# Kernel optimization log

Measured on AMD Instinct MI355X. Metric: run time of the kernel, lower is better.

Reference implementation:

```python
import jax, jax.numpy as jnp
import numpy as np

D = 128       # in_features
H = 256       # hidden
OUT = 128     # out_features
NUM_STEPS = 3
K = 8         # k_neighbors (k = min(K, N))


def setup_inputs() -> dict:
    key = jax.random.key(0)
    ks = jax.random.split(key, 12)
    s = 0.02
    return {
        "x":    jax.random.normal(ks[0], (4, 4096, D), dtype=jnp.float32),
        # neighbor_proj: Linear(D -> H)
        "Wn":   jax.random.normal(ks[1], (D, H), dtype=jnp.float32) * s,
        "bn":   jnp.zeros((H,), dtype=jnp.float32),
        # local_rule[0]: Linear(D + H -> H)
        "W1":   jax.random.normal(ks[2], (D + H, H), dtype=jnp.float32) * s,
        "b1":   jnp.zeros((H,), dtype=jnp.float32),
        # local_rule[1]: LayerNorm(H)
        "ln_g": jnp.ones((H,), dtype=jnp.float32),
        "ln_b": jnp.zeros((H,), dtype=jnp.float32),
        # local_rule[3]: Linear(H -> D)
        "W2":   jax.random.normal(ks[3], (H, D), dtype=jnp.float32) * s,
        "b2":   jnp.zeros((D,), dtype=jnp.float32),
        # out_proj: Linear(D -> OUT)
        "Wo":   jax.random.normal(ks[4], (D, OUT), dtype=jnp.float32) * s,
        "bo":   jnp.zeros((OUT,), dtype=jnp.float32),
    }


def _layernorm(h, g, b, eps=1e-5):
    mu = jnp.mean(h, axis=-1, keepdims=True)
    var = jnp.var(h, axis=-1, keepdims=True)
    return (h - mu) * jax.lax.rsqrt(var + eps) * g + b


def reference(x, Wn, bn, W1, b1, ln_g, ln_b, W2, b2, Wo, bo):
    B, N, _ = x.shape
    k = min(K, N)
    batch_ix = jnp.arange(B)[:, None, None]  # (B,1,1)
    state = x
    for _ in range(NUM_STEPS):
        keys = state @ Wn + bn                                     # (B,N,H)
        keys = keys / jnp.maximum(
            jnp.linalg.norm(keys, axis=-1, keepdims=True), 1e-12)  # F.normalize
        sim = jnp.einsum('bnh,bmh->bnm', keys, keys)               # (B,N,N)
        _, idx = jax.lax.top_k(sim, k)                             # (B,N,k)
        gathered = state[batch_ix, idx]                            # (B,N,k,D)
        neighbor_agg = gathered.mean(axis=2) @ Wn + bn             # (B,N,H)
        combined = jnp.concatenate([state, neighbor_agg], axis=-1) # (B,N,D+H)
        h = _layernorm(combined @ W1 + b1, ln_g, ln_b)
        update = jax.nn.silu(h) @ W2 + b2                          # (B,N,D)
        state = state + update
    return state.mean(axis=1) @ Wo + bo                            # (B,OUT)
```

## Files before the change

kernel.cpp:

```cpp
#include <hip/hip_runtime.h>

#define DDIM 128
#define HDIM 256
#define BQ   4
#define NN   4096
#define RTOT (BQ*NN)

typedef short short8 __attribute__((ext_vector_type(8)));
typedef short short4v __attribute__((ext_vector_type(4)));
typedef float f32x16 __attribute__((ext_vector_type(16)));

__device__ inline unsigned short f2bf(float f) {
    unsigned int u = __float_as_uint(f);
    unsigned int r = (u + 0x7fffu + ((u >> 16) & 1u)) >> 16;
    return (unsigned short)r;
}
__device__ inline float bf2f(unsigned short h) {
    return __uint_as_float(((unsigned int)h) << 16);
}

#define MFMA32(a, b, c) __builtin_amdgcn_mfma_f32_32x32x16_bf16(a, b, c, 0, 0, 0)

__global__ void pack_w_kernel(const float* __restrict__ W, int N,
                              unsigned short* __restrict__ ph, unsigned short* __restrict__ pl) {
    int l = threadIdx.x, l31 = l & 31, lh = l >> 5;
    int nt = N >> 5;
    int t = blockIdx.x / nt, c = blockIdx.x % nt;
    short8 hv, lv;
#pragma unroll
    for (int j = 0; j < 8; ++j) {
        float f = W[(size_t)(t * 16 + lh * 8 + j) * N + c * 32 + l31];
        unsigned short h = f2bf(f);
        hv[j] = (short)h;
        lv[j] = (short)f2bf(f - bf2f(h));
    }
    *(short8*)(ph + (size_t)(blockIdx.x * 64 + l) * 8) = hv;
    *(short8*)(pl + (size_t)(blockIdx.x * 64 + l) * 8) = lv;
}

__global__ __launch_bounds__(256, 2)
void sim_topk_kernel(const unsigned short* __restrict__ khi,
                     const unsigned short* __restrict__ klo,
                     int* __restrict__ idxout) {
    __shared__ __align__(16) char smem[4 * 4 * 4096];

    const int id = blockIdx.x;
    const int xcd = id & 7;
    const int b = xcd >> 1;
    const int j = ((id >> 3) << 1) | (xcd & 1);
    const int rowbase = j * 32;
    const unsigned short* khiB = khi + (size_t)b * NN * HDIM;
    const unsigned short* kloB = klo + (size_t)b * NN * HDIM;

    const int tid = threadIdx.x;
    const int lane = tid & 63, w = tid >> 6;
    const int l31 = lane & 31, lh = lane >> 5;

    short8 ah[16], al[16];
    {
        const unsigned short* ph = khiB + (size_t)(rowbase + l31) * HDIM + lh * 8;
        const unsigned short* pl = kloB + (size_t)(rowbase + l31) * HDIM + lh * 8;
#pragma unroll
        for (int T = 0; T < 16; ++T) {
            ah[T] = *(const short8*)(ph + T * 16);
            al[T] = *(const short8*)(pl + T * 16);
        }
    }
#pragma unroll
    for (int T = 0; T < 16; ++T) {
        asm volatile("" : "+v"(ah[T]));
        asm volatile("" : "+v"(al[T]));
    }

    char* mybuf = smem + w * 16384;

    const int sc = lane >> 2, sg = lane & 3;
    const int ssw = (sg ^ ((sc >> 1) & 3)) * 8;
    auto stage = [&](int s) {
        const int cs2 = s >> 3, ks2 = s & 7;
        char* dst = mybuf + (s % 4) * 4096;
        const int c0 = w * 1024 + cs2 * 32;
#pragma unroll
        for (int p = 0; p < 2; ++p) {
            const unsigned short* pb = p ? kloB : khiB;
#pragma unroll
            for (int i = 0; i < 2; ++i) {
                const unsigned short* src = pb + (size_t)(c0 + i * 16 + sc) * HDIM + ks2 * 32 + ssw;
                __builtin_amdgcn_global_load_lds(
                    (const __attribute__((address_space(1))) void*)src,
                    (__attribute__((address_space(3))) void*)(dst + p * 2048 + i * 1024), 16, 0, 0);
            }
        }
    };

    stage(0);
    stage(1);
    stage(2);

    const int key = (l31 >> 1) & 3;
    const int rb0 = l31 * 64 + ((lh ^ key) * 16);
    const int rb1 = l31 * 64 + (((2 + lh) ^ key) * 16);

    float tv[8]; int ti[8];
#pragma unroll
    for (int s = 0; s < 8; ++s) { tv[s] = -1e30f; ti[s] = 0x7fffffff; }

    for (int cs = 0; cs < 32; ++cs) {
        f32x16 acc;
#pragma unroll
        for (int r = 0; r < 16; ++r) acc[r] = 0.f;

#pragma unroll
        for (int ks = 0; ks < 8; ++ks) {
            const int s = cs * 8 + ks;
            if (s < 254)       asm volatile("s_waitcnt vmcnt(8)" ::: "memory");
            else if (s == 254) asm volatile("s_waitcnt vmcnt(4)" ::: "memory");
            else               asm volatile("s_waitcnt vmcnt(0)" ::: "memory");

            const char* bufc = mybuf + (s % 4) * 4096;
            short8 Bh0 = *(const short8*)(bufc + rb0);
            short8 Bl0 = *(const short8*)(bufc + 2048 + rb0);
            short8 Bh1 = *(const short8*)(bufc + rb1);
            short8 Bl1 = *(const short8*)(bufc + 2048 + rb1);
            asm volatile("s_waitcnt lgkmcnt(4)" ::: "memory");
            if (s + 3 < 256) stage(s + 3);

            const int T0 = ks * 2, T1 = ks * 2 + 1;
            acc = MFMA32(Bh0, ah[T0], acc);
            acc = MFMA32(Bh0, al[T0], acc);
            acc = MFMA32(Bl0, ah[T0], acc);
            acc = MFMA32(Bh1, ah[T1], acc);
            acc = MFMA32(Bh1, al[T1], acc);
            acc = MFMA32(Bl1, ah[T1], acc);
        }

        const int cbase = w * 1024 + cs * 32 + 4 * lh;
#pragma unroll
        for (int r = 0; r < 16; ++r) {
            float v = acc[r];
            int col = cbase + (r & 3) + 8 * (r >> 2);
            if (v > tv[7]) {
                tv[7] = v; ti[7] = col;
#pragma unroll
                for (int q = 7; q >= 1; --q) {
                    if (tv[q] > tv[q - 1]) {
                        float a0 = tv[q]; tv[q] = tv[q - 1]; tv[q - 1] = a0;
                        int   c0_ = ti[q]; ti[q] = ti[q - 1]; ti[q - 1] = c0_;
                    }
                }
            }
        }
    }

    __syncthreads();
    float* vbuf = (float*)smem;
    int*   ibuf = (int*)(smem + 32 * 66 * 4);
    const int list = w * 2 + lh;
#pragma unroll
    for (int s = 0; s < 8; ++s) {
        vbuf[l31 * 66 + list * 8 + s] = tv[s];
        ibuf[l31 * 66 + list * 8 + s] = ti[s];
    }
    __syncthreads();
    if (tid < 32) {
        float fv[8]; int fi[8];
#pragma unroll
        for (int s = 0; s < 8; ++s) { fv[s] = -1e30f; fi[s] = 0x7fffffff; }
        for (int e = 0; e < 64; ++e) {
            float v = vbuf[tid * 66 + e];
            int  ix = ibuf[tid * 66 + e];
            bool ins = (v > fv[7]) || (v == fv[7] && ix < fi[7]);
            if (ins) {
                fv[7] = v; fi[7] = ix;
#pragma unroll
                for (int q = 7; q >= 1; --q) {
                    bool sw = (fv[q] > fv[q - 1]) || (fv[q] == fv[q - 1] && fi[q] < fi[q - 1]);
                    if (sw) {
                        float a0 = fv[q]; fv[q] = fv[q - 1]; fv[q - 1] = a0;
                        int   c0_ = fi[q]; fi[q] = fi[q - 1]; fi[q - 1] = c0_;
                    }
                }
            }
        }
        size_t basei = ((size_t)b * NN + rowbase + tid) * 8;
#pragma unroll
        for (int s = 0; s < 8; ++s) idxout[basei + s] = fi[s];
    }
}

__global__ __launch_bounds__(256, 2)
void gemm_keys_mfma(const float* __restrict__ A,
                    const unsigned short* __restrict__ wh, const unsigned short* __restrict__ wl,
                    const float* __restrict__ bias,
                    unsigned short* __restrict__ khi, unsigned short* __restrict__ klo) {
    __shared__ float ssqbuf[2][32][2];
    const int tid = threadIdx.x, lane = tid & 63, w = tid >> 6;
    const int l31 = lane & 31, lh = lane >> 5;
    const int rw = w & 1, cw = w >> 1;
    const int row = blockIdx.x * 64 + rw * 32 + l31;

    short8 ahi[8], alo[8];
    const float* ap = A + (size_t)row * DDIM + lh * 8;
#pragma unroll
    for (int T = 0; T < 8; ++T) {
        float4 f0 = *(const float4*)(ap + T * 16);
        float4 f1 = *(const float4*)(ap + T * 16 + 4);
        float ff[8] = {f0.x, f0.y, f0.z, f0.w, f1.x, f1.y, f1.z, f1.w};
#pragma unroll
        for (int j2 = 0; j2 < 8; ++j2) {
            unsigned short h = f2bf(ff[j2]);
            ahi[T][j2] = (short)h;
            alo[T][j2] = (short)f2bf(ff[j2] - bf2f(h));
        }
    }

    f32x16 acc[4];
#pragma unroll
    for (int ct = 0; ct < 4; ++ct)
#pragma unroll
        for (int r = 0; r < 16; ++r) acc[ct][r] = 0.f;

#pragma unroll
    for (int T = 0; T < 8; ++T) {
#pragma unroll
        for (int ct = 0; ct < 4; ++ct) {
            const size_t pi = (size_t)((T * 8 + cw * 4 + ct) * 64 + lane) * 8;
            short8 bh = *(const short8*)(wh + pi);
            short8 bl = *(const short8*)(wl + pi);
            acc[ct] = MFMA32(bh, ahi[T], acc[ct]);
            acc[ct] = MFMA32(bl, ahi[T], acc[ct]);
            acc[ct] = MFMA32(bh, alo[T], acc[ct]);
        }
    }

    float ss = 0.f;
#pragma unroll
    for (int ct = 0; ct < 4; ++ct)
#pragma unroll
        for (int g = 0; g < 4; ++g) {
            const int c0 = cw * 128 + ct * 32 + g * 8 + lh * 4;
            float4 bz = *(const float4*)(bias + c0);
            float bzf[4] = {bz.x, bz.y, bz.z, bz.w};
#pragma unroll
            for (int j2 = 0; j2 < 4; ++j2) {
                acc[ct][g * 4 + j2] += bzf[j2];
                ss += acc[ct][g * 4 + j2] * acc[ct][g * 4 + j2];
            }
        }
    ss += __shfl_xor(ss, 32);
    if (lh == 0) ssqbuf[rw][l31][cw] = ss;
    __syncthreads();
    float sstot = ssqbuf[rw][l31][0] + ssqbuf[rw][l31][1];
    float scn = 1.0f / fmaxf(sqrtf(sstot), 1e-12f);

#pragma unroll
    for (int ct = 0; ct < 4; ++ct)
#pragma unroll
        for (int g = 0; g < 4; ++g) {
            const int c0 = cw * 128 + ct * 32 + g * 8 + lh * 4;
            short4v hv, lv;
#pragma unroll
            for (int j2 = 0; j2 < 4; ++j2) {
                float vn = acc[ct][g * 4 + j2] * scn;
                unsigned short h = f2bf(vn);
                hv[j2] = (short)h;
                lv[j2] = (short)f2bf(vn - bf2f(h));
            }
            *(short4v*)(khi + (size_t)row * HDIM + c0) = hv;
            *(short4v*)(klo + (size_t)row * HDIM + c0) = lv;
        }
}

__global__ __launch_bounds__(256, 2)
void gemm_agg_mfma(const float* __restrict__ A,
                   const unsigned short* __restrict__ wh, const unsigned short* __restrict__ wl,
                   const float* __restrict__ bias,
                   unsigned short* __restrict__ oh, unsigned short* __restrict__ ol) {
    const int tid = threadIdx.x, lane = tid & 63, w = tid >> 6;
    const int l31 = lane & 31, lh = lane >> 5;
    const int rw = w & 1, cw = w >> 1;
    const int row = blockIdx.x * 64 + rw * 32 + l31;

    short8 ahi[8], alo[8];
    const float* ap = A + (size_t)row * DDIM + lh * 8;
#pragma unroll
    for (int T = 0; T < 8; ++T) {
        float4 f0 = *(const float4*)(ap + T * 16);
        float4 f1 = *(const float4*)(ap + T * 16 + 4);
        float ff[8] = {f0.x, f0.y, f0.z, f0.w, f1.x, f1.y, f1.z, f1.w};
#pragma unroll
        for (int j2 = 0; j2 < 8; ++j2) {
            unsigned short h = f2bf(ff[j2]);
            ahi[T][j2] = (short)h;
            alo[T][j2] = (short)f2bf(ff[j2] - bf2f(h));
        }
    }

    f32x16 acc[4];
#pragma unroll
    for (int ct = 0; ct < 4; ++ct)
#pragma unroll
        for (int r = 0; r < 16; ++r) acc[ct][r] = 0.f;

#pragma unroll
    for (int T = 0; T < 8; ++T) {
#pragma unroll
        for (int ct = 0; ct < 4; ++ct) {
            const size_t pi = (size_t)((T * 8 + cw * 4 + ct) * 64 + lane) * 8;
            short8 bh = *(const short8*)(wh + pi);
            short8 bl = *(const short8*)(wl + pi);
            acc[ct] = MFMA32(bh, ahi[T], acc[ct]);
            acc[ct] = MFMA32(bl, ahi[T], acc[ct]);
            acc[ct] = MFMA32(bh, alo[T], acc[ct]);
        }
    }

#pragma unroll
    for (int ct = 0; ct < 4; ++ct)
#pragma unroll
        for (int g = 0; g < 4; ++g) {
            const int c0 = cw * 128 + ct * 32 + g * 8 + lh * 4;
            float4 bz = *(const float4*)(bias + c0);
            float bzf[4] = {bz.x, bz.y, bz.z, bz.w};
            short4v hv, lv;
#pragma unroll
            for (int j2 = 0; j2 < 4; ++j2) {
                float vn = acc[ct][g * 4 + j2] + bzf[j2];
                unsigned short h = f2bf(vn);
                hv[j2] = (short)h;
                lv[j2] = (short)f2bf(vn - bf2f(h));
            }
            *(short4v*)(oh + (size_t)row * HDIM + c0) = hv;
            *(short4v*)(ol + (size_t)row * HDIM + c0) = lv;
        }
}

__global__ __launch_bounds__(256, 2)
void gemm_ln_mfma(const float* __restrict__ state,
                  const unsigned short* __restrict__ agh, const unsigned short* __restrict__ agl,
                  const unsigned short* __restrict__ wh, const unsigned short* __restrict__ wl,
                  const float* __restrict__ b1, const float* __restrict__ lng,
                  const float* __restrict__ lnb,
                  unsigned short* __restrict__ gh, unsigned short* __restrict__ gl) {
    __shared__ float s1buf[2][32][2], s2buf[2][32][2];
    const int tid = threadIdx.x, lane = tid & 63, w = tid >> 6;
    const int l31 = lane & 31, lh = lane >> 5;
    const int rw = w & 1, cw = w >> 1;
    const int row = blockIdx.x * 64 + rw * 32 + l31;

    f32x16 acc[4];
#pragma unroll
    for (int ct = 0; ct < 4; ++ct)
#pragma unroll
        for (int r = 0; r < 16; ++r) acc[ct][r] = 0.f;

    short8 ahi[8], alo[8];
    {
        const float* ap = state + (size_t)row * DDIM + lh * 8;
#pragma unroll
        for (int T = 0; T < 8; ++T) {
            float4 f0 = *(const float4*)(ap + T * 16);
            float4 f1 = *(const float4*)(ap + T * 16 + 4);
            float ff[8] = {f0.x, f0.y, f0.z, f0.w, f1.x, f1.y, f1.z, f1.w};
#pragma unroll
            for (int j2 = 0; j2 < 8; ++j2) {
                unsigned short h = f2bf(ff[j2]);
                ahi[T][j2] = (short)h;
                alo[T][j2] = (short)f2bf(ff[j2] - bf2f(h));
            }
        }
#pragma unroll
        for (int T = 0; T < 8; ++T)
#pragma unroll
            for (int ct = 0; ct < 4; ++ct) {
                const size_t pi = (size_t)((T * 8 + cw * 4 + ct) * 64 + lane) * 8;
                short8 bh = *(const short8*)(wh + pi);
                short8 bl = *(const short8*)(wl + pi);
                acc[ct] = MFMA32(bh, ahi[T], acc[ct]);
                acc[ct] = MFMA32(bl, ahi[T], acc[ct]);
                acc[ct] = MFMA32(bh, alo[T], acc[ct]);
            }
    }
#pragma unroll
    for (int kc = 1; kc < 3; ++kc) {
#pragma unroll
        for (int T = 0; T < 8; ++T) {
            ahi[T] = *(const short8*)(agh + (size_t)row * HDIM + (kc - 1) * 128 + T * 16 + lh * 8);
            alo[T] = *(const short8*)(agl + (size_t)row * HDIM + (kc - 1) * 128 + T * 16 + lh * 8);
        }
#pragma unroll
        for (int T = 0; T < 8; ++T)
#pragma unroll
            for (int ct = 0; ct < 4; ++ct) {
                const size_t pi = (size_t)(((kc * 8 + T) * 8 + cw * 4 + ct) * 64 + lane) * 8;
                short8 bh = *(const short8*)(wh + pi);
                short8 bl = *(const short8*)(wl + pi);
                acc[ct] = MFMA32(bh, ahi[T], acc[ct]);
                acc[ct] = MFMA32(bl, ahi[T], acc[ct]);
                acc[ct] = MFMA32(bh, alo[T], acc[ct]);
            }
    }

    float s1 = 0.f, s2 = 0.f;
#pragma unroll
    for (int ct = 0; ct < 4; ++ct)
#pragma unroll
        for (int g = 0; g < 4; ++g) {
            const int c0 = cw * 128 + ct * 32 + g * 8 + lh * 4;
            float4 bz = *(const float4*)(b1 + c0);
            float bzf[4] = {bz.x, bz.y, bz.z, bz.w};
#pragma unroll
            for (int j2 = 0; j2 < 4; ++j2) {
                acc[ct][g * 4 + j2] += bzf[j2];
                s1 += acc[ct][g * 4 + j2];
                s2 += acc[ct][g * 4 + j2] * acc[ct][g * 4 + j2];
            }
        }
    s1 += __shfl_xor(s1, 32);
    s2 += __shfl_xor(s2, 32);
    if (lh == 0) { s1buf[rw][l31][cw] = s1; s2buf[rw][l31][cw] = s2; }
    __syncthreads();
    float s1t = s1buf[rw][l31][0] + s1buf[rw][l31][1];
    float s2t = s2buf[rw][l31][0] + s2buf[rw][l31][1];
    float mu = s1t * (1.0f / HDIM);
    float var = s2t * (1.0f / HDIM) - mu * mu;
    float inv = 1.0f / sqrtf(var + 1e-5f);

#pragma unroll
    for (int ct = 0; ct < 4; ++ct)
#pragma unroll
        for (int g = 0; g < 4; ++g) {
            const int c0 = cw * 128 + ct * 32 + g * 8 + lh * 4;
            float4 gg = *(const float4*)(lng + c0);
            float4 bb = *(const float4*)(lnb + c0);
            float ggf[4] = {gg.x, gg.y, gg.z, gg.w};
            float bbf[4] = {bb.x, bb.y, bb.z, bb.w};
            short4v hv, lv;
#pragma unroll
            for (int j2 = 0; j2 < 4; ++j2) {
                float hval = (acc[ct][g * 4 + j2] - mu) * inv * ggf[j2] + bbf[j2];
                float gval = hval / (1.0f + expf(-hval));
                unsigned short h = f2bf(gval);
                hv[j2] = (short)h;
                lv[j2] = (short)f2bf(gval - bf2f(h));
            }
            *(short4v*)(gh + (size_t)row * HDIM + c0) = hv;
            *(short4v*)(gl + (size_t)row * HDIM + c0) = lv;
        }
}

__global__ __launch_bounds__(256, 2)
void gemm_upd_mfma(const unsigned short* __restrict__ gh, const unsigned short* __restrict__ gl,
                   const unsigned short* __restrict__ wh, const unsigned short* __restrict__ wl,
                   const float* __restrict__ b2, float* __restrict__ state) {
    const int tid = threadIdx.x, lane = tid & 63, w = tid >> 6;
    const int l31 = lane & 31, lh = lane >> 5;
    const int rw = w & 1, cw = w >> 1;
    const int row = blockIdx.x * 64 + rw * 32 + l31;

    f32x16 acc[2];
#pragma unroll
    for (int ct = 0; ct < 2; ++ct)
#pragma unroll
        for (int r = 0; r < 16; ++r) acc[ct][r] = 0.f;

    short8 ahi[8], alo[8];
#pragma unroll
    for (int kc = 0; kc < 2; ++kc) {
#pragma unroll
        for (int T = 0; T < 8; ++T) {
            ahi[T] = *(const short8*)(gh + (size_t)row * HDIM + kc * 128 + T * 16 + lh * 8);
            alo[T] = *(const short8*)(gl + (size_t)row * HDIM + kc * 128 + T * 16 + lh * 8);
        }
#pragma unroll
        for (int T = 0; T < 8; ++T)
#pragma unroll
            for (int ct = 0; ct < 2; ++ct) {
                const size_t pi = (size_t)(((kc * 8 + T) * 4 + cw * 2 + ct) * 64 + lane) * 8;
                short8 bh = *(const short8*)(wh + pi);
                short8 bl = *(const short8*)(wl + pi);
                acc[ct] = MFMA32(bh, ahi[T], acc[ct]);
                acc[ct] = MFMA32(bl, ahi[T], acc[ct]);
                acc[ct] = MFMA32(bh, alo[T], acc[ct]);
            }
    }

#pragma unroll
    for (int ct = 0; ct < 2; ++ct)
#pragma unroll
        for (int g = 0; g < 4; ++g) {
            const int c0 = cw * 64 + ct * 32 + g * 8 + lh * 4;
            float4 bz = *(const float4*)(b2 + c0);
            float bzf[4] = {bz.x, bz.y, bz.z, bz.w};
            float4* sp = (float4*)(state + (size_t)row * DDIM + c0);
            float4 sv = *sp;
            float svf[4] = {sv.x, sv.y, sv.z, sv.w};
#pragma unroll
            for (int j2 = 0; j2 < 4; ++j2) svf[j2] += acc[ct][g * 4 + j2] + bzf[j2];
            sv.x = svf[0]; sv.y = svf[1]; sv.z = svf[2]; sv.w = svf[3];
            *sp = sv;
        }
}

__global__ void gather_mean_kernel(const float* __restrict__ state, const int* __restrict__ idx,
                                   float* __restrict__ M) {
    __shared__ int ilds[16];
    int tid = threadIdx.x;
    int row0 = blockIdx.x * 2;
    if (tid < 16) ilds[tid] = idx[(size_t)row0 * 8 + tid];
    __syncthreads();
    int lr = tid >> 7, d = tid & 127;
    int grow = row0 + lr;
    int b = grow >> 12;
    const float* sb = state + (size_t)b * NN * DDIM;
    float acc = 0.f;
#pragma unroll
    for (int k = 0; k < 8; ++k) acc += sb[(size_t)ilds[lr * 8 + k] * DDIM + d];
    M[(size_t)grow * DDIM + d] = acc * 0.125f;
}

__global__ void partial_mean_kernel(const float* __restrict__ state, float* __restrict__ partial) {
    int b = blockIdx.y, seg = blockIdx.x, tid = threadIdx.x;
    const float* sp = state + ((size_t)b * NN + (size_t)seg * 128) * DDIM;
    float acc = 0.f;
    for (int i = 0; i < 128; ++i) acc += sp[(size_t)i * DDIM + tid];
    partial[((size_t)b * 32 + seg) * DDIM + tid] = acc;
}

__global__ void final_out_kernel(const float* __restrict__ partial, const float* __restrict__ Wo,
                                 const float* __restrict__ bo, float* __restrict__ out) {
    __shared__ float mean[BQ][DDIM];
    int tid = threadIdx.x;
    for (int o = tid; o < BQ * DDIM; o += 256) {
        int b = o >> 7, d = o & 127;
        float s = 0.f;
        for (int p = 0; p < 32; ++p) s += partial[((size_t)b * 32 + p) * DDIM + d];
        mean[b][d] = s * (1.0f / NN);
    }
    __syncthreads();
    for (int o = tid; o < BQ * DDIM; o += 256) {
        int b = o >> 7, c = o & 127;
        float acc = bo[c];
        for (int d = 0; d < DDIM; ++d) acc += mean[b][d] * Wo[d * DDIM + c];
        out[o] = acc;
    }
}

extern "C" void kernel_launch(void* const* d_in, const int* in_sizes, int n_in,
                              void* d_out, int out_size, void* d_ws, size_t ws_size,
                              hipStream_t stream) {
    const float* x   = (const float*)d_in[0];
    const float* Wn  = (const float*)d_in[1];
    const float* bn  = (const float*)d_in[2];
    const float* W1  = (const float*)d_in[3];
    const float* b1  = (const float*)d_in[4];
    const float* lng = (const float*)d_in[5];
    const float* lnb = (const float*)d_in[6];
    const float* W2  = (const float*)d_in[7];
    const float* b2  = (const float*)d_in[8];
    const float* Wo  = (const float*)d_in[9];
    const float* bo  = (const float*)d_in[10];
    float* out = (float*)d_out;

    float* ws    = (float*)d_ws;
    float* state = ws;
    unsigned short* agghi = (unsigned short*)(state + (size_t)RTOT * DDIM);
    unsigned short* agglo = agghi + (size_t)RTOT * HDIM;
    unsigned short* khi_b = agglo + (size_t)RTOT * HDIM;
    unsigned short* klo_b = khi_b + (size_t)RTOT * HDIM;
    float* Mbuf = (float*)khi_b;
    unsigned short* ghi = khi_b;
    unsigned short* glo = klo_b;
    float* partial = (float*)(klo_b + (size_t)RTOT * HDIM);
    int*   idxbuf  = (int*)(partial + (size_t)BQ * 32 * DDIM);
    unsigned short* wnh = (unsigned short*)(idxbuf + (size_t)RTOT * 8);
    unsigned short* wnl = wnh + 128 * 256;
    unsigned short* w1h = wnl + 128 * 256;
    unsigned short* w1l = w1h + 384 * 256;
    unsigned short* w2h = w1l + 384 * 256;
    unsigned short* w2l = w2h + 256 * 128;

    hipMemcpyAsync(state, x, (size_t)RTOT * DDIM * sizeof(float),
                   hipMemcpyDeviceToDevice, stream);

    pack_w_kernel<<<(128 / 16) * (256 / 32), 64, 0, stream>>>(Wn, 256, wnh, wnl);
    pack_w_kernel<<<(384 / 16) * (256 / 32), 64, 0, stream>>>(W1, 256, w1h, w1l);
    pack_w_kernel<<<(256 / 16) * (128 / 32), 64, 0, stream>>>(W2, 128, w2h, w2l);

    for (int step = 0; step < 3; ++step) {
        gemm_keys_mfma<<<RTOT / 64, 256, 0, stream>>>(state, wnh, wnl, bn, khi_b, klo_b);
        sim_topk_kernel<<<512, 256, 0, stream>>>(khi_b, klo_b, idxbuf);
        gather_mean_kernel<<<RTOT / 2, 256, 0, stream>>>(state, idxbuf, Mbuf);
        gemm_agg_mfma<<<RTOT / 64, 256, 0, stream>>>(Mbuf, wnh, wnl, bn, agghi, agglo);
        gemm_ln_mfma<<<RTOT / 64, 256, 0, stream>>>(state, agghi, agglo, w1h, w1l,
                                                    b1, lng, lnb, ghi, glo);
        gemm_upd_mfma<<<RTOT / 64, 256, 0, stream>>>(ghi, glo, w2h, w2l, b2, state);
    }
    partial_mean_kernel<<<dim3(32, BQ), 128, 0, stream>>>(state, partial);
    final_out_kernel<<<1, 256, 0, stream>>>(partial, Wo, bo, out);
}
```

Measured before the change: 832.2 us.

## Fuse gather-mean into aggregate GEMM and restage sim LDS tiles with 64-wide swizzle

Removes the separate gather_mean kernel and its M buffer round-trip. The aggregate GEMM now reads the eight neighbor indices per row and sums the neighbor state rows directly while building its bf16 hi/lo operands. Separately, the sim/top-k kernel's LDS staging is reorganized so that each stage loads either the hi or the lo half of a 64-wide k slab, using an 8-way XOR swizzle. Stages then alternate between 8 MFMAs (hi stage) and 4 MFMAs (lo stage) instead of 6 per stage. The fused gather adds scattered global reads inside the GEMM, and the new staging changes the load pipeline's balance.

After: 863.3 us. 3.7% more time.

```diff
diff --git a/kernel.cpp b/kernel.cpp
--- a/kernel.cpp
+++ b/kernel.cpp
@@ -74,22 +74,20 @@
 
     char* mybuf = smem + w * 16384;
 
-    const int sc = lane >> 2, sg = lane & 3;
-    const int ssw = (sg ^ ((sc >> 1) & 3)) * 8;
+    const int sc8 = lane >> 3, sg8 = lane & 7;
     auto stage = [&](int s) {
-        const int cs2 = s >> 3, ks2 = s & 7;
-        char* dst = mybuf + (s % 4) * 4096;
+        const int cs2 = s >> 3, sub = s & 7;
+        const int kb2 = sub >> 1;
+        const unsigned short* pb = (sub & 1) ? kloB : khiB;
+        char* dst = mybuf + (s & 3) * 4096;
         const int c0 = w * 1024 + cs2 * 32;
 #pragma unroll
-        for (int p = 0; p < 2; ++p) {
-            const unsigned short* pb = p ? kloB : khiB;
-#pragma unroll
-            for (int i = 0; i < 2; ++i) {
-                const unsigned short* src = pb + (size_t)(c0 + i * 16 + sc) * HDIM + ks2 * 32 + ssw;
-                __builtin_amdgcn_global_load_lds(
-                    (const __attribute__((address_space(1))) void*)src,
-                    (__attribute__((address_space(3))) void*)(dst + p * 2048 + i * 1024), 16, 0, 0);
-            }
+        for (int i = 0; i < 4; ++i) {
+            const unsigned short* src =
+                pb + (size_t)(c0 + i * 8 + sc8) * HDIM + kb2 * 64 + ((sg8 ^ sc8) * 8);
+            __builtin_amdgcn_global_load_lds(
+                (const __attribute__((address_space(1))) void*)src,
+                (__attribute__((address_space(3))) void*)(dst + i * 1024), 16, 0, 0);
         }
     };
 
@@ -97,9 +95,12 @@
     stage(1);
     stage(2);
 
-    const int key = (l31 >> 1) & 3;
-    const int rb0 = l31 * 64 + ((lh ^ key) * 16);
-    const int rb1 = l31 * 64 + (((2 + lh) ^ key) * 16);
+    const int key = l31 & 7;
+    const int rbase = l31 * 128;
+    const int sl0 = (((0) * 2 + lh) ^ key) * 16;
+    const int sl1 = (((1) * 2 + lh) ^ key) * 16;
+    const int sl2 = (((2) * 2 + lh) ^ key) * 16;
+    const int sl3 = (((3) * 2 + lh) ^ key) * 16;
 
     float tv[8]; int ti[8];
 #pragma unroll
@@ -111,27 +112,36 @@
         for (int r = 0; r < 16; ++r) acc[r] = 0.f;
 
 #pragma unroll
-        for (int ks = 0; ks < 8; ++ks) {
-            const int s = cs * 8 + ks;
+        for (int sub = 0; sub < 8; ++sub) {
+            const int s = cs * 8 + sub;
             if (s < 254)       asm volatile("s_waitcnt vmcnt(8)" ::: "memory");
             else if (s == 254) asm volatile("s_waitcnt vmcnt(4)" ::: "memory");
             else               asm volatile("s_waitcnt vmcnt(0)" ::: "memory");
 
-            const char* bufc = mybuf + (s % 4) * 4096;
-            short8 Bh0 = *(const short8*)(bufc + rb0);
-            short8 Bl0 = *(const short8*)(bufc + 2048 + rb0);
-            short8 Bh1 = *(const short8*)(bufc + rb1);
-            short8 Bl1 = *(const short8*)(bufc + 2048 + rb1);
+            const char* bufc = mybuf + (s & 3) * 4096;
+            short8 B0 = *(const short8*)(bufc + rbase + sl0);
+            short8 B1 = *(const short8*)(bufc + rbase + sl1);
+            short8 B2 = *(const short8*)(bufc + rbase + sl2);
+            short8 B3 = *(const short8*)(bufc + rbase + sl3);
             asm volatile("s_waitcnt lgkmcnt(4)" ::: "memory");
             if (s + 3 < 256) stage(s + 3);
 
-            const int T0 = ks * 2, T1 = ks * 2 + 1;
-            acc = MFMA32(Bh0, ah[T0], acc);
-            acc = MFMA32(Bh0, al[T0], acc);
-            acc = MFMA32(Bl0, ah[T0], acc);
-            acc = MFMA32(Bh1, ah[T1], acc);
-            acc = MFMA32(Bh1, al[T1], acc);
-            acc = MFMA32(Bl1, ah[T1], acc);
+            const int T0 = (sub >> 1) * 4;
+            if ((sub & 1) == 0) {
+                acc = MFMA32(B0, ah[T0],     acc);
+                acc = MFMA32(B0, al[T0],     acc);
+                acc = MFMA32(B1, ah[T0 + 1], acc);
+                acc = MFMA32(B1, al[T0 + 1], acc);
+                acc = MFMA32(B2, ah[T0 + 2], acc);
+                acc = MFMA32(B2, al[T0 + 2], acc);
+                acc = MFMA32(B3, ah[T0 + 3], acc);
+                acc = MFMA32(B3, al[T0 + 3], acc);
+            } else {
+                acc = MFMA32(B0, ah[T0],     acc);
+                acc = MFMA32(B1, ah[T0 + 1], acc);
+                acc = MFMA32(B2, ah[T0 + 2], acc);
+                acc = MFMA32(B3, ah[T0 + 3], acc);
+            }
         }
 
         const int cbase = w * 1024 + cs * 32 + 4 * lh;
@@ -272,7 +282,7 @@
 }
 
 __global__ __launch_bounds__(256, 2)
-void gemm_agg_mfma(const float* __restrict__ A,
+void gemm_agg_mfma(const float* __restrict__ state, const int* __restrict__ idx,
                    const unsigned short* __restrict__ wh, const unsigned short* __restrict__ wl,
                    const float* __restrict__ bias,
                    unsigned short* __restrict__ oh, unsigned short* __restrict__ ol) {
@@ -280,19 +290,32 @@
     const int l31 = lane & 31, lh = lane >> 5;
     const int rw = w & 1, cw = w >> 1;
     const int row = blockIdx.x * 64 + rw * 32 + l31;
+    const int bb = row >> 12;
+    const float* sb = state + (size_t)bb * NN * DDIM;
+    const int* mi = idx + (size_t)row * 8;
+
+    int ridx[8];
+#pragma unroll
+    for (int k = 0; k < 8; ++k) ridx[k] = mi[k];
 
     short8 ahi[8], alo[8];
-    const float* ap = A + (size_t)row * DDIM + lh * 8;
 #pragma unroll
     for (int T = 0; T < 8; ++T) {
-        float4 f0 = *(const float4*)(ap + T * 16);
-        float4 f1 = *(const float4*)(ap + T * 16 + 4);
-        float ff[8] = {f0.x, f0.y, f0.z, f0.w, f1.x, f1.y, f1.z, f1.w};
+        float fr[8] = {0.f, 0.f, 0.f, 0.f, 0.f, 0.f, 0.f, 0.f};
+#pragma unroll
+        for (int k = 0; k < 8; ++k) {
+            const float* rp = sb + (size_t)ridx[k] * DDIM + T * 16 + lh * 8;
+            float4 f0 = *(const float4*)rp;
+            float4 f1 = *(const float4*)(rp + 4);
+            fr[0] += f0.x; fr[1] += f0.y; fr[2] += f0.z; fr[3] += f0.w;
+            fr[4] += f1.x; fr[5] += f1.y; fr[6] += f1.z; fr[7] += f1.w;
+        }
 #pragma unroll
         for (int j2 = 0; j2 < 8; ++j2) {
-            unsigned short h = f2bf(ff[j2]);
+            float v = fr[j2] * 0.125f;
+            unsigned short h = f2bf(v);
             ahi[T][j2] = (short)h;
-            alo[T][j2] = (short)f2bf(ff[j2] - bf2f(h));
+            alo[T][j2] = (short)f2bf(v - bf2f(h));
         }
     }
 
@@ -500,23 +523,6 @@
             sv.x = svf[0]; sv.y = svf[1]; sv.z = svf[2]; sv.w = svf[3];
             *sp = sv;
         }
-}
-
-__global__ void gather_mean_kernel(const float* __restrict__ state, const int* __restrict__ idx,
-                                   float* __restrict__ M) {
-    __shared__ int ilds[16];
-    int tid = threadIdx.x;
-    int row0 = blockIdx.x * 2;
-    if (tid < 16) ilds[tid] = idx[(size_t)row0 * 8 + tid];
-    __syncthreads();
-    int lr = tid >> 7, d = tid & 127;
-    int grow = row0 + lr;
-    int b = grow >> 12;
-    const float* sb = state + (size_t)b * NN * DDIM;
-    float acc = 0.f;
-#pragma unroll
-    for (int k = 0; k < 8; ++k) acc += sb[(size_t)ilds[lr * 8 + k] * DDIM + d];
-    M[(size_t)grow * DDIM + d] = acc * 0.125f;
 }
 
 __global__ void partial_mean_kernel(const float* __restrict__ state, float* __restrict__ partial) {
@@ -568,7 +574,6 @@
     unsigned short* agglo = agghi + (size_t)RTOT * HDIM;
     unsigned short* khi_b = agglo + (size_t)RTOT * HDIM;
     unsigned short* klo_b = khi_b + (size_t)RTOT * HDIM;
-    float* Mbuf = (float*)khi_b;
     unsigned short* ghi = khi_b;
     unsigned short* glo = klo_b;
     float* partial = (float*)(klo_b + (size_t)RTOT * HDIM);
@@ -590,8 +595,7 @@
     for (int step = 0; step < 3; ++step) {
         gemm_keys_mfma<<<RTOT / 64, 256, 0, stream>>>(state, wnh, wnl, bn, khi_b, klo_b);
         sim_topk_kernel<<<512, 256, 0, stream>>>(khi_b, klo_b, idxbuf);
-        gather_mean_kernel<<<RTOT / 2, 256, 0, stream>>>(state, idxbuf, Mbuf);
-        gemm_agg_mfma<<<RTOT / 64, 256, 0, stream>>>(Mbuf, wnh, wnl, bn, agghi, agglo);
+        gemm_agg_mfma<<<RTOT / 64, 256, 0, stream>>>(state, idxbuf, wnh, wnl, bn, agghi, agglo);
         gemm_ln_mfma<<<RTOT / 64, 256, 0, stream>>>(state, agghi, agglo, w1h, w1l,
                                                     b1, lng, lnb, ghi, glo);
         gemm_upd_mfma<<<RTOT / 64, 256, 0, stream>>>(ghi, glo, w2h, w2l, b2, state);
```
